# Optimization experiments

Hardware: AMD Instinct MI355X
Metric: run time of the kernel (lower is better)

The kernel has to match this reference:

```python
import jax, jax.numpy as jnp
import numpy as np

C = 1000      # num_classes
U = 10        # proxies_per_class
D = 512       # feature_dim
B = 4096      # batch
ALPHA = 32.0
DELTA = 0.1


def _l2norm(x, axis=-1):
    return x / jnp.linalg.norm(x, axis=axis, keepdims=True).clip(1e-12)


def setup_inputs() -> dict:
    key = jax.random.key(0)
    k1, k2, k3 = jax.random.split(key, 3)
    features = jax.random.normal(k1, (B, D), dtype=jnp.float32)
    labels = jax.random.randint(k2, (B,), 0, C)
    # proxies are initialized to row-normalized gaussians (as in __init__)
    proxies = _l2norm(jax.random.normal(k3, (C * U, D), dtype=jnp.float32))
    return {"features": features, "labels": labels, "proxies": proxies}


def reference(features, labels, proxies):
    # proxy_class_ids: [C*U], class id of each proxy
    class_ids = jnp.repeat(jnp.arange(C), U)

    x = _l2norm(features)          # [B, D]
    p = _l2norm(proxies)           # [P, D], P = C*U
    sim = x @ p.T                  # [B, P]

    # ---- infer_logits, agg='soft', tau=1 ----
    s = sim.reshape(B, C, U)       # per-class proxy similarities
    w = jax.nn.softmax(s, axis=2)
    logits = jnp.sum(w * s, axis=2)  # [B, C], tau=1 so no extra scaling

    # ---- _compute_proxy_loss (Proxy-Anchor) ----
    sim_t = sim.T                                         # [P, B]
    pos_mask = labels[None, :] == class_ids[:, None]      # [P, B]
    neg_inf = jnp.finfo(jnp.float32).min
    z_pos = jnp.where(pos_mask, -ALPHA * (sim_t - DELTA), neg_inf)
    z_neg = jnp.where(pos_mask, neg_inf, ALPHA * (sim_t + DELTA))
    lse_pos = jax.nn.logsumexp(z_pos, axis=1)             # [P]
    lse_neg = jax.nn.logsumexp(z_neg, axis=1)             # [P]
    pos_term = jax.nn.softplus(lse_pos)
    neg_term = jax.nn.softplus(lse_neg)
    has_pos = pos_mask.any(axis=1)
    pos_loss = jnp.where(has_pos, pos_term, 0.0).sum() / jnp.maximum(
        has_pos.sum(), 1).astype(jnp.float32)
    neg_loss = neg_term.mean()
    proxy_loss = pos_loss + neg_loss

    return logits, proxy_loss
```

## Files before the change

kernel.cpp:

```cpp
#include <hip/hip_runtime.h>
#include <hip/hip_bf16.h>

#define C_CLS   1000
#define U_PX    10
#define D_DIM   512
#define B_BATCH 4096
#define P_PX    (C_CLS * U_PX)
#define ALPHA_F 32.0f
#define DELTA_F 0.1f

#define BM 256
#define BN 80
#define BK 64
#define SIMP 84

#define A_OFF   0
#define B_OFF   32768
#define SMEM_SZ 43008

typedef __attribute__((ext_vector_type(8))) short bf16x8;
typedef __attribute__((ext_vector_type(4))) float f32x4;

typedef __attribute__((address_space(1))) const void gv_t;
typedef __attribute__((address_space(3))) void lv_t;

__device__ __forceinline__ void gload_lds16(const void* g, void* lds) {
    __builtin_amdgcn_global_load_lds((gv_t*)g, (lv_t*)lds, 16, 0, 0);
}

__device__ __forceinline__ unsigned int f2bf(float f) {
    union { float f; unsigned u; } c; c.f = f;
    unsigned u = c.u;
    return (u + 0x7FFF + ((u >> 16) & 1)) >> 16;
}

__global__ __launch_bounds__(256) void norm_rows_kernel(const float* __restrict__ feat,
                                                        const float* __restrict__ prox,
                                                        unsigned int* __restrict__ xout,
                                                        unsigned int* __restrict__ pout) {
    const int wid  = threadIdx.x >> 6;
    const int lane = threadIdx.x & 63;
    int row = blockIdx.x * 4 + wid;
    const float* in;
    unsigned int* out;
    if (row < B_BATCH) { in = feat + (size_t)row * D_DIM;   out = xout + (size_t)row * (D_DIM / 2); }
    else { row -= B_BATCH; in = prox + (size_t)row * D_DIM; out = pout + (size_t)row * (D_DIM / 2); }
    const float4 v0 = reinterpret_cast<const float4*>(in)[lane * 2];
    const float4 v1 = reinterpret_cast<const float4*>(in)[lane * 2 + 1];
    float ss = v0.x*v0.x + v0.y*v0.y + v0.z*v0.z + v0.w*v0.w
             + v1.x*v1.x + v1.y*v1.y + v1.z*v1.z + v1.w*v1.w;
    #pragma unroll
    for (int off = 1; off < 64; off <<= 1) ss += __shfl_xor(ss, off, 64);
    const float inv = 1.0f / fmaxf(sqrtf(ss), 1e-12f);
    uint4 o;
    o.x = f2bf(v0.x * inv) | (f2bf(v0.y * inv) << 16);
    o.y = f2bf(v0.z * inv) | (f2bf(v0.w * inv) << 16);
    o.z = f2bf(v1.x * inv) | (f2bf(v1.y * inv) << 16);
    o.w = f2bf(v1.z * inv) | (f2bf(v1.w * inv) << 16);
    *reinterpret_cast<uint4*>(out + lane * 4) = o;
}

__global__ __launch_bounds__(256, 3) void fused_gemm_kernel(
    const unsigned short* __restrict__ xbf,
    const unsigned short* __restrict__ pbf,
    const int*            __restrict__ labels,
    float*                __restrict__ logits,
    double*               __restrict__ pos_sum,
    double*               __restrict__ neg_sum)
{
    __shared__ __align__(16) char smem[SMEM_SZ];
    __shared__ int lab_lds[BM];

    const int t    = threadIdx.x;
    const int m0   = blockIdx.x * BM;
    const int n0   = blockIdx.y * BN;
    const int wid  = t >> 6;
    const int lane = t & 63;
    const int l15  = lane & 15;
    const int kgrp = lane >> 4;

    if (t < BM) lab_lds[t] = labels[m0 + t];

    const int srow = lane >> 3;
    const int scol = (lane & 7) ^ srow;

    const int koff0 = ((kgrp    ) ^ (l15 & 7)) << 4;
    const int koff1 = ((kgrp + 4) ^ (l15 & 7)) << 4;

    f32x4 acc[4][5];
    #pragma unroll
    for (int m = 0; m < 4; ++m)
        #pragma unroll
        for (int n = 0; n < 5; ++n) acc[m][n] = (f32x4){0.f, 0.f, 0.f, 0.f};

    for (int ks = 0; ks < D_DIM / BK; ++ks) {
        const int kbase = ks * BK;
        #pragma unroll
        for (int c = wid; c < 32; c += 4)
            gload_lds16(xbf + (size_t)(m0 + c * 8 + srow) * D_DIM + kbase + scol * 8,
                        smem + A_OFF + c * 1024);
        for (int c = wid; c < 10; c += 4)
            gload_lds16(pbf + (size_t)(n0 + c * 8 + srow) * D_DIM + kbase + scol * 8,
                        smem + B_OFF + c * 1024);
        __syncthreads();
        __builtin_amdgcn_s_setprio(1);
        #pragma unroll
        for (int kk8 = 0; kk8 < 2; ++kk8) {
            const int koff = kk8 ? koff1 : koff0;
            bf16x8 b[5];
            #pragma unroll
            for (int n = 0; n < 5; ++n)
                b[n] = *reinterpret_cast<const bf16x8*>(smem + B_OFF + (n * 16 + l15) * 128 + koff);
            #pragma unroll
            for (int m = 0; m < 4; ++m) {
                const bf16x8 a = *reinterpret_cast<const bf16x8*>(
                    smem + A_OFF + (wid * 64 + m * 16 + l15) * 128 + koff);
                #pragma unroll
                for (int n = 0; n < 5; ++n)
                    acc[m][n] = __builtin_amdgcn_mfma_f32_16x16x32_bf16(a, b[n], acc[m][n], 0, 0, 0);
            }
        }
        __builtin_amdgcn_s_setprio(0);
        __syncthreads();
    }

    {
        int labv[16];
        #pragma unroll
        for (int m = 0; m < 4; ++m)
            #pragma unroll
            for (int r = 0; r < 4; ++r)
                labv[m * 4 + r] = lab_lds[wid * 64 + m * 16 + kgrp * 4 + r];
        #pragma unroll
        for (int n = 0; n < 5; ++n) {
            const int col = n * 16 + l15;
            const int cls = (n0 + col) / U_PX;
            float pos = 0.f, neg = 0.f;
            #pragma unroll
            for (int m = 0; m < 4; ++m)
                #pragma unroll
                for (int r = 0; r < 4; ++r) {
                    const float s = acc[m][n][r];
                    const bool isp = (labv[m * 4 + r] == cls);
                    const float e = __expf(isp ? (-ALPHA_F * (s - DELTA_F))
                                               : ( ALPHA_F * (s + DELTA_F)));
                    if (isp) pos += e; else neg += e;
                }
            pos += __shfl_xor(pos, 16, 64); pos += __shfl_xor(pos, 32, 64);
            neg += __shfl_xor(neg, 16, 64); neg += __shfl_xor(neg, 32, 64);
            if (lane < 16) {
                atomicAdd(&neg_sum[n0 + col], (double)neg);
                if (pos != 0.f) atomicAdd(&pos_sum[n0 + col], (double)pos);
            }
        }
    }

    float* simw = reinterpret_cast<float*>(smem) + wid * (16 * SIMP);
    #pragma unroll
    for (int m = 0; m < 4; ++m) {
        #pragma unroll
        for (int n = 0; n < 5; ++n)
            #pragma unroll
            for (int r = 0; r < 4; ++r)
                simw[(kgrp * 4 + r) * SIMP + n * 16 + l15] = acc[m][n][r];
        #pragma unroll
        for (int it = 0; it < 2; ++it) {
            const int j   = lane + it * 64;
            const int r   = j >> 3;
            const int c   = j & 7;
            const float* s = simw + r * SIMP + c * U_PX;
            float wsum = 0.f, wssum = 0.f;
            #pragma unroll
            for (int u = 0; u < U_PX; ++u) {
                const float sv = s[u];
                const float e = __expf(sv);
                wsum += e; wssum += e * sv;
            }
            logits[(size_t)(m0 + wid * 64 + m * 16 + r) * C_CLS + (n0 / U_PX + c)] = wssum / wsum;
        }
        __builtin_amdgcn_s_waitcnt(0);
    }
}

__global__ __launch_bounds__(1024) void finalize_kernel(
    const double* __restrict__ pos_sum,
    const double* __restrict__ neg_sum,
    float*        __restrict__ out_loss)
{
    __shared__ double sp[1024], sn[1024];
    __shared__ int    sc[1024];
    const int t = threadIdx.x;
    double pAcc = 0.0, nAcc = 0.0; int cnt = 0;
    for (int p = t; p < P_PX; p += 1024) {
        nAcc += log1p(neg_sum[p]);
        const double ps = pos_sum[p];
        if (ps != 0.0) { pAcc += log1p(ps); cnt++; }
    }
    sp[t] = pAcc; sn[t] = nAcc; sc[t] = cnt;
    __syncthreads();
    for (int s = 512; s > 0; s >>= 1) {
        if (t < s) { sp[t] += sp[t + s]; sn[t] += sn[t + s]; sc[t] += sc[t + s]; }
        __syncthreads();
    }
    if (t == 0)
        out_loss[0] = (float)(sp[0] / (double)max(sc[0], 1) + sn[0] / (double)P_PX);
}

extern "C" void kernel_launch(void* const* d_in, const int* in_sizes, int n_in,
                              void* d_out, int out_size, void* d_ws, size_t ws_size,
                              hipStream_t stream) {
    const float* features = (const float*)d_in[0];
    const int*   labels   = (const int*)d_in[1];
    const float* proxies  = (const float*)d_in[2];
    float* out = (float*)d_out;

    char* ws = (char*)d_ws;
    unsigned short* xbf = (unsigned short*)ws;
    unsigned short* pbf = (unsigned short*)(ws + (size_t)B_BATCH * D_DIM * 2);
    double* pos_sum = (double*)(ws + (size_t)(B_BATCH + P_PX) * D_DIM * 2);
    double* neg_sum = pos_sum + P_PX;

    hipMemsetAsync(pos_sum, 0, 2 * P_PX * sizeof(double), stream);

    norm_rows_kernel<<<(B_BATCH + P_PX) / 4, 256, 0, stream>>>(
        features, proxies, (unsigned int*)xbf, (unsigned int*)pbf);

    fused_gemm_kernel<<<dim3(B_BATCH / BM, P_PX / BN), 256, 0, stream>>>(
        xbf, pbf, labels, out, pos_sum, neg_sum);

    finalize_kernel<<<1, 1024, 0, stream>>>(pos_sum, neg_sum,
                                            out + (size_t)B_BATCH * C_CLS);
}
```

Baseline: 104.8 us.

## Fold buffer zeroing into norm kernel and finalize via last-block reduction

Removes the separate memset launch by having the normalization kernel zero the accumulation buffers and block counter. Also removes the standalone finalize kernel: the last GEMM block to finish, detected with an atomic counter after a threadfence, reads the accumulated sums and computes the loss. This cuts two launches and their gaps, in exchange for a serial tail in one block of 256 threads and an atomic per block.

```diff
diff --git a/kernel.cpp b/kernel.cpp
--- a/kernel.cpp
+++ b/kernel.cpp
@@ -13,10 +13,13 @@
 #define BN 80
 #define BK 64
 #define SIMP 84
+#define NBLK ((B_BATCH / BM) * (P_PX / BN))
 
 #define A_OFF   0
 #define B_OFF   32768
 #define SMEM_SZ 43008
+
+#define ZERO_DBL (2 * P_PX + 4)
 
 typedef __attribute__((ext_vector_type(8))) short bf16x8;
 typedef __attribute__((ext_vector_type(4))) float f32x4;
@@ -37,7 +40,11 @@
 __global__ __launch_bounds__(256) void norm_rows_kernel(const float* __restrict__ feat,
                                                         const float* __restrict__ prox,
                                                         unsigned int* __restrict__ xout,
-                                                        unsigned int* __restrict__ pout) {
+                                                        unsigned int* __restrict__ pout,
+                                                        double* __restrict__ zbase) {
+    const int zidx = blockIdx.x * 256 + threadIdx.x;
+    if (zidx < ZERO_DBL) zbase[zidx] = 0.0;
+
     const int wid  = threadIdx.x >> 6;
     const int lane = threadIdx.x & 63;
     int row = blockIdx.x * 4 + wid;
@@ -66,10 +73,13 @@
     const int*            __restrict__ labels,
     float*                __restrict__ logits,
     double*               __restrict__ pos_sum,
-    double*               __restrict__ neg_sum)
+    double*               __restrict__ neg_sum,
+    double*               __restrict__ accum,
+    float*                __restrict__ out_loss)
 {
     __shared__ __align__(16) char smem[SMEM_SZ];
     __shared__ int lab_lds[BM];
+    __shared__ unsigned lastFlag;
 
     const int t    = threadIdx.x;
     const int m0   = blockIdx.x * BM;
@@ -180,30 +190,37 @@
         }
         __builtin_amdgcn_s_waitcnt(0);
     }
-}
-
-__global__ __launch_bounds__(1024) void finalize_kernel(
-    const double* __restrict__ pos_sum,
-    const double* __restrict__ neg_sum,
-    float*        __restrict__ out_loss)
-{
-    __shared__ double sp[1024], sn[1024];
-    __shared__ int    sc[1024];
-    const int t = threadIdx.x;
-    double pAcc = 0.0, nAcc = 0.0; int cnt = 0;
-    for (int p = t; p < P_PX; p += 1024) {
-        nAcc += log1p(neg_sum[p]);
-        const double ps = pos_sum[p];
-        if (ps != 0.0) { pAcc += log1p(ps); cnt++; }
-    }
-    sp[t] = pAcc; sn[t] = nAcc; sc[t] = cnt;
+
     __syncthreads();
-    for (int s = 512; s > 0; s >>= 1) {
-        if (t < s) { sp[t] += sp[t + s]; sn[t] += sn[t + s]; sc[t] += sc[t + s]; }
+    __threadfence();
+    if (t == 0)
+        lastFlag = (atomicAdd((unsigned*)(accum + 3), 1u) == NBLK - 1);
+    __syncthreads();
+    if (lastFlag) {
+        double pAcc = 0.0, nAcc = 0.0; int cnt = 0;
+        for (int p = t; p < P_PX; p += 256) {
+            const double nsv = atomicAdd(&neg_sum[p], 0.0);
+            nAcc += log1p(nsv);
+            const double psv = atomicAdd(&pos_sum[p], 0.0);
+            if (psv != 0.0) { pAcc += log1p(psv); cnt++; }
+        }
+        #pragma unroll
+        for (int off = 1; off < 64; off <<= 1) {
+            pAcc += __shfl_xor(pAcc, off, 64);
+            nAcc += __shfl_xor(nAcc, off, 64);
+            cnt  += __shfl_xor(cnt,  off, 64);
+        }
+        double* sred = reinterpret_cast<double*>(smem);
+        int*    cred = reinterpret_cast<int*>(smem + 64);
+        if (lane == 0) { sred[wid] = pAcc; sred[4 + wid] = nAcc; cred[wid] = cnt; }
         __syncthreads();
-    }
-    if (t == 0)
-        out_loss[0] = (float)(sp[0] / (double)max(sc[0], 1) + sn[0] / (double)P_PX);
+        if (t == 0) {
+            const double a0 = sred[0] + sred[1] + sred[2] + sred[3];
+            const double a1 = sred[4] + sred[5] + sred[6] + sred[7];
+            const int  csum = cred[0] + cred[1] + cred[2] + cred[3];
+            out_loss[0] = (float)(a0 / (double)max(csum, 1) + a1 / (double)P_PX);
+        }
+    }
 }
 
 extern "C" void kernel_launch(void* const* d_in, const int* in_sizes, int n_in,
@@ -219,15 +236,12 @@
     unsigned short* pbf = (unsigned short*)(ws + (size_t)B_BATCH * D_DIM * 2);
     double* pos_sum = (double*)(ws + (size_t)(B_BATCH + P_PX) * D_DIM * 2);
     double* neg_sum = pos_sum + P_PX;
-
-    hipMemsetAsync(pos_sum, 0, 2 * P_PX * sizeof(double), stream);
+    double* accum   = neg_sum + P_PX;
 
     norm_rows_kernel<<<(B_BATCH + P_PX) / 4, 256, 0, stream>>>(
-        features, proxies, (unsigned int*)xbf, (unsigned int*)pbf);
+        features, proxies, (unsigned int*)xbf, (unsigned int*)pbf, pos_sum);
 
     fused_gemm_kernel<<<dim3(B_BATCH / BM, P_PX / BN), 256, 0, stream>>>(
-        xbf, pbf, labels, out, pos_sum, neg_sum);
-
-    finalize_kernel<<<1, 1024, 0, stream>>>(pos_sum, neg_sum,
-                                            out + (size_t)B_BATCH * C_CLS);
-}
+        xbf, pbf, labels, out, pos_sum, neg_sum, accum,
+        out + (size_t)B_BATCH * C_CLS);
+}
```

Result: slower. 308.4 us (+194.4%).
